# Optimization experiments

Hardware: AMD Instinct MI355X
Metric: run time of the kernel (lower is better)

Reference implementation:

```python
import jax, jax.numpy as jnp
import numpy as np

N, D, H, E, OUT, TOP_K = 16384, 1024, 4096, 8, 4096, 2


def setup_inputs() -> dict:
    key = jax.random.key(0)
    ks = jax.random.split(key, 9)
    s_d = 1.0 / np.sqrt(D)
    s_h = 1.0 / np.sqrt(H)
    return {
        "x": jax.random.normal(ks[0], (N, D), dtype=jnp.float32),
        "W_in": jax.random.normal(ks[1], (D, D), dtype=jnp.float32) * s_d,
        "b_in": jax.random.normal(ks[2], (D,), dtype=jnp.float32) * 0.01,
        "W_gate": jax.random.normal(ks[3], (D, E), dtype=jnp.float32) * s_d,
        "W1": jax.random.normal(ks[4], (E, D, H), dtype=jnp.float32) * s_d,
        "b1": jax.random.normal(ks[5], (E, H), dtype=jnp.float32) * 0.01,
        "W2": jax.random.normal(ks[6], (E, H, D), dtype=jnp.float32) * s_h,
        "b2": jax.random.normal(ks[7], (E, D), dtype=jnp.float32) * 0.01,
        "W_head": jax.random.normal(ks[8], (D, OUT), dtype=jnp.float32) * s_d,
    }


def reference(x, W_in, b_in, W_gate, W1, b1, W2, b2, W_head):
    # Input linear: [N, D]
    h = x @ W_in + b_in

    # Gating: softmax over experts, keep top-k, renormalize
    probs = jax.nn.softmax(h @ W_gate, axis=-1)            # [N, E]
    top_vals, top_idx = jax.lax.top_k(probs, TOP_K)        # [N, K]
    top_vals = top_vals / jnp.sum(top_vals, axis=-1, keepdims=True)
    rows = jnp.arange(h.shape[0])[:, None]
    combine = jnp.zeros_like(probs).at[rows, top_idx].set(top_vals)  # [N, E]

    # Expert FFNs, weighted combine (loop over small fixed expert count)
    moe_out = jnp.zeros_like(h)
    for e in range(E):
        he = jax.nn.relu(h @ W1[e] + b1[e])                # [N, H]
        ye = he @ W2[e] + b2[e]                            # [N, D]
        moe_out = moe_out + combine[:, e:e + 1] * ye

    # Head (no bias)
    return moe_out @ W_head
```

## Files before the change

### kernel.cpp

```cpp
#include <hip/hip_runtime.h>
#include <math.h>

#define NN 16384
#define DD 1024
#define HH 4096
#define EE 8
#define OUTD 4096

typedef unsigned short u16;
typedef short v8s __attribute__((ext_vector_type(8)));
typedef float v4f __attribute__((ext_vector_type(4)));

__device__ __forceinline__ u16 f2bf(float f) {
    unsigned int u = __float_as_uint(f);
    u = (u + 0x7fffu + ((u >> 16) & 1u)) >> 16;
    return (u16)u;
}

__device__ __forceinline__ void cp16(const u16* g, u16* l) {
    __builtin_amdgcn_global_load_lds(
        (const __attribute__((address_space(1))) unsigned int*)g,
        (__attribute__((address_space(3))) unsigned int*)l, 16, 0, 0);
}

__global__ __launch_bounds__(256) void cvt_bf16(const float* __restrict__ in,
                                                u16* __restrict__ out, int n4) {
    int i = blockIdx.x * 256 + threadIdx.x;
    if (i < n4) {
        float4 v = ((const float4*)in)[i];
        ushort4 o;
        o.x = f2bf(v.x); o.y = f2bf(v.y); o.z = f2bf(v.z); o.w = f2bf(v.w);
        ((ushort4*)out)[i] = o;
    }
}

__global__ __launch_bounds__(256) void transpose_cast(const float* __restrict__ in,
                                                      u16* __restrict__ out,
                                                      int rows, int cols) {
    __shared__ float t[32][33];
    const float* inp = in + (size_t)blockIdx.z * rows * cols;
    u16* outp = out + (size_t)blockIdx.z * rows * cols;
    int c0 = blockIdx.x * 32, r0 = blockIdx.y * 32;
    int tx = threadIdx.x & 31, ty = threadIdx.x >> 5;
#pragma unroll
    for (int i = 0; i < 4; ++i)
        t[ty + i * 8][tx] = inp[(size_t)(r0 + ty + i * 8) * cols + c0 + tx];
    __syncthreads();
#pragma unroll
    for (int i = 0; i < 4; ++i)
        outp[(size_t)(c0 + ty + i * 8) * rows + r0 + tx] = f2bf(t[tx][ty + i * 8]);
}

__global__ __launch_bounds__(256) void compute_G(const float* __restrict__ Win,
                                                 const float* __restrict__ Wg,
                                                 const float* __restrict__ b_in,
                                                 float* __restrict__ Gt,
                                                 float* __restrict__ cvec) {
    int tid = blockIdx.x * 256 + threadIdx.x;
    if (tid < EE * DD) {
        int e = tid >> 10, d = tid & 1023;
        float s = 0.f;
        for (int j = 0; j < DD; ++j) s += Win[(size_t)d * DD + j] * Wg[j * EE + e];
        Gt[e * DD + d] = s;
    } else if (tid < EE * DD + EE) {
        int e = tid - EE * DD;
        float s = 0.f;
        for (int j = 0; j < DD; ++j) s += b_in[j] * Wg[j * EE + e];
        cvec[e] = s;
    }
}

__global__ __launch_bounds__(256) void gate_kernel(const float* __restrict__ x,
                                                   const float* __restrict__ Gt,
                                                   const float* __restrict__ cvec,
                                                   int* __restrict__ counts,
                                                   int* __restrict__ toklist,
                                                   float* __restrict__ wtlist) {
    int wave = threadIdx.x >> 6, lane = threadIdx.x & 63;
    int t = blockIdx.x * 4 + wave;
    const float* xr = x + (size_t)t * DD;
    float p[EE];
#pragma unroll
    for (int e = 0; e < EE; ++e) p[e] = 0.f;
    for (int it = 0; it < DD / 64; ++it) {
        int d = it * 64 + lane;
        float xv = xr[d];
#pragma unroll
        for (int e = 0; e < EE; ++e) p[e] += xv * Gt[e * DD + d];
    }
#pragma unroll
    for (int e = 0; e < EE; ++e) {
        float v = p[e];
#pragma unroll
        for (int m = 32; m >= 1; m >>= 1) v += __shfl_xor(v, m);
        p[e] = v;
    }
    if (lane == 0) {
        float l[EE];
#pragma unroll
        for (int e = 0; e < EE; ++e) l[e] = p[e] + cvec[e];
        int i0 = 0; float v0 = l[0];
#pragma unroll
        for (int e = 1; e < EE; ++e) if (l[e] > v0) { v0 = l[e]; i0 = e; }
        int i1 = -1; float v1 = -1e30f;
#pragma unroll
        for (int e = 0; e < EE; ++e) if (e != i0 && l[e] > v1) { v1 = l[e]; i1 = e; }
        float e1 = __expf(v1 - v0);
        float inv = 1.f / (1.f + e1);
        float w0 = inv, w1 = e1 * inv;
        int pos0 = atomicAdd(&counts[i0], 1);
        toklist[i0 * NN + pos0] = t; wtlist[i0 * NN + pos0] = w0;
        int pos1 = atomicAdd(&counts[i1], 1);
        toklist[i1 * NN + pos1] = t; wtlist[i1 * NN + pos1] = w1;
    }
}

__global__ void offsets_kernel(const int* __restrict__ counts, int* __restrict__ offs) {
    if (threadIdx.x == 0) {
        int a = 0;
        for (int e = 0; e < EE; ++e) { offs[e] = a; a += counts[e]; }
    }
}

template <int MODE, int K, int LDC>
__global__ __launch_bounds__(256, 2) void gemm_bt(
    const u16* __restrict__ A, const u16* __restrict__ Btb,
    u16* __restrict__ outb, float* __restrict__ outf,
    const float* __restrict__ biasb,
    const int* __restrict__ toklist, const float* __restrict__ wtlist,
    const int* __restrict__ counts, const int* __restrict__ offsets,
    float* __restrict__ moe) {
    __shared__ __align__(16) u16 As[3][128 * 32];
    __shared__ __align__(16) u16 Bs[3][128 * 32];

    constexpr int GX = (MODE == 1 || MODE == 2) ? EE * 128 : NN / 128;
    constexpr int GY = LDC / 128;
    constexpr int NWG = GX * GY;
    constexpr int QC = NWG / 8;
    static_assert(NWG % 8 == 0, "xcd swizzle needs nwg%8==0");

    const int wg = blockIdx.x + GX * blockIdx.y;
    const int lid = (wg & 7) * QC + (wg >> 3);
    const int bx = lid & (GX - 1);
    const int by = lid / GX;

    int e = 0, mt = bx, cnt = 0, ofs = 0;
    if (MODE == 1 || MODE == 2) {
        e = bx >> 7; mt = bx & 127;
        cnt = counts[e];
        if (mt * 128 >= cnt) return;
        ofs = offsets[e];
    }
    const int m0 = mt * 128;
    const int n0 = by * 128;

    const u16* Bt = Btb;
    const float* bias = biasb;
    if (MODE == 1) { Bt += (size_t)e * HH * DD; bias += e * HH; }
    if (MODE == 2) { Bt += (size_t)e * DD * HH; bias += e * DD; }

    const int lane = threadIdx.x & 63;
    const int wave = threadIdx.x >> 6;
    const int rl = lane >> 2;
    const int kc = lane & 3;
    const int kcs = kc ^ ((rl >> 1) & 3);

    const u16* aS[2];
    const u16* bS[2];
#pragma unroll
    for (int s = 0; s < 2; ++s) {
        int trow = wave * 32 + s * 16 + rl;
        long arow;
        if (MODE == 1) {
            int rr = m0 + trow; if (rr >= cnt) rr = cnt - 1;
            arow = toklist[e * NN + rr];
        } else if (MODE == 2) {
            int rr = m0 + trow; if (rr >= cnt) rr = cnt - 1;
            arow = ofs + rr;
        } else {
            arow = m0 + trow;
        }
        aS[s] = A + (size_t)arow * K + kcs * 8;
        bS[s] = Bt + (size_t)(n0 + trow) * K + kcs * 8;
    }
    u16* aL[2] = { &As[0][(wave * 32) * 32], &As[0][(wave * 32 + 16) * 32] };
    u16* bL[2] = { &Bs[0][(wave * 32) * 32], &Bs[0][(wave * 32 + 16) * 32] };

    const int wm = wave & 1, wn = wave >> 1;
    const int fr = lane & 15;
    const int kswz = ((lane >> 4) ^ ((fr >> 1) & 3)) * 8;

    v4f acc[4][4];
#pragma unroll
    for (int i = 0; i < 4; ++i)
#pragma unroll
        for (int j = 0; j < 4; ++j)
#pragma unroll
            for (int c = 0; c < 4; ++c) acc[i][j][c] = 0.f;

    auto STAGE = [&](int kt, int buf) {
#pragma unroll
        for (int s = 0; s < 2; ++s) {
            cp16(aS[s] + kt * 32, aL[s] + buf * 4096);
            cp16(bS[s] + kt * 32, bL[s] + buf * 4096);
        }
    };

    constexpr int NIT = K / 32;
    STAGE(0, 0);
    STAGE(1, 1);

    int cur = 0, pre = 2;
    for (int it = 0; it < NIT; ++it) {
        if (it + 2 < NIT) {
            STAGE(it + 2, pre);
            asm volatile("s_waitcnt vmcnt(8)" ::: "memory");
        } else if (it + 2 == NIT) {
            asm volatile("s_waitcnt vmcnt(4)" ::: "memory");
        } else {
            asm volatile("s_waitcnt vmcnt(0)" ::: "memory");
        }
        __builtin_amdgcn_s_barrier();
        asm volatile("" ::: "memory");

        v8s af[4], bv[4];
#pragma unroll
        for (int i = 0; i < 4; ++i)
            af[i] = *(const v8s*)&As[cur][(wm * 64 + i * 16 + fr) * 32 + kswz];
#pragma unroll
        for (int j = 0; j < 4; ++j)
            bv[j] = *(const v8s*)&Bs[cur][(wn * 64 + j * 16 + fr) * 32 + kswz];

        __builtin_amdgcn_s_setprio(1);
#pragma unroll
        for (int i = 0; i < 4; ++i)
#pragma unroll
            for (int j = 0; j < 4; ++j)
                acc[i][j] = __builtin_amdgcn_mfma_f32_16x16x32_bf16(af[i], bv[j], acc[i][j], 0, 0, 0);
        __builtin_amdgcn_s_setprio(0);

        asm volatile("" ::: "memory");
        __builtin_amdgcn_s_barrier();
        cur = cur == 2 ? 0 : cur + 1;
        pre = pre == 2 ? 0 : pre + 1;
    }

    const int quad = (lane >> 4) * 4;
#pragma unroll
    for (int i = 0; i < 4; ++i) {
#pragma unroll
        for (int r = 0; r < 4; ++r) {
            int rloc = wm * 64 + i * 16 + quad + r;
            int grow = m0 + rloc;
            if ((MODE == 1 || MODE == 2) && grow >= cnt) continue;
            int tok = 0; float wgt = 0.f;
            if (MODE == 2) { tok = toklist[e * NN + grow]; wgt = wtlist[e * NN + grow]; }
#pragma unroll
            for (int j = 0; j < 4; ++j) {
                int col = n0 + wn * 64 + j * 16 + fr;
                float v = acc[i][j][r];
                if (MODE == 0) {
                    outb[(size_t)grow * LDC + col] = f2bf(v + bias[col]);
                } else if (MODE == 1) {
                    float t = v + bias[col];
                    t = t > 0.f ? t : 0.f;
                    outb[(size_t)(ofs + grow) * LDC + col] = f2bf(t);
                } else if (MODE == 2) {
                    atomicAdd(&moe[(size_t)tok * LDC + col], wgt * (v + bias[col]));
                } else {
                    outf[(size_t)grow * LDC + col] = v;
                }
            }
        }
    }
}

extern "C" void kernel_launch(void* const* d_in, const int* in_sizes, int n_in,
                              void* d_out, int out_size, void* d_ws, size_t ws_size,
                              hipStream_t stream) {
    const float* x    = (const float*)d_in[0];
    const float* Win  = (const float*)d_in[1];
    const float* b_in = (const float*)d_in[2];
    const float* Wg   = (const float*)d_in[3];
    const float* W1   = (const float*)d_in[4];
    const float* b1   = (const float*)d_in[5];
    const float* W2   = (const float*)d_in[6];
    const float* b2   = (const float*)d_in[7];
    const float* Wh   = (const float*)d_in[8];
    float* out = (float*)d_out;

    char* p = (char*)d_ws;
    size_t off = 0;
    auto alloc = [&](size_t bytes) {
        char* r = p + off;
        off = (off + bytes + 255) & ~(size_t)255;
        return r;
    };
    u16*   x_bf   = (u16*)alloc((size_t)NN * DD * 2);
    u16*   wint   = (u16*)alloc((size_t)DD * DD * 2);
    u16*   w1t    = (u16*)alloc((size_t)EE * DD * HH * 2);
    u16*   w2t    = (u16*)alloc((size_t)EE * DD * HH * 2);
    u16*   wht    = (u16*)alloc((size_t)DD * OUTD * 2);
    u16*   h_bf   = (u16*)alloc((size_t)NN * DD * 2);
    float* moe_f  = (float*)alloc((size_t)NN * DD * 4);
    u16*   moe_bf = (u16*)alloc((size_t)NN * DD * 2);
    float* Gt     = (float*)alloc((size_t)EE * DD * 4);
    float* cvec   = (float*)alloc(256);
    int*   counts = (int*)alloc(256);
    int*   offs   = (int*)alloc(256);
    int*   tok    = (int*)alloc((size_t)EE * NN * 4);
    float* wt     = (float*)alloc((size_t)EE * NN * 4);
    if (off > ws_size) return;

    u16* he = (u16*)d_out;

    hipMemsetAsync(counts, 0, 256, stream);
    hipMemsetAsync(moe_f, 0, (size_t)NN * DD * 4, stream);

    cvt_bf16<<<dim3(NN * DD / 4 / 256), 256, 0, stream>>>(x, x_bf, NN * DD / 4);
    transpose_cast<<<dim3(DD / 32, DD / 32, 1), 256, 0, stream>>>(Win, wint, DD, DD);
    transpose_cast<<<dim3(HH / 32, DD / 32, EE), 256, 0, stream>>>(W1, w1t, DD, HH);
    transpose_cast<<<dim3(DD / 32, HH / 32, EE), 256, 0, stream>>>(W2, w2t, HH, DD);
    transpose_cast<<<dim3(OUTD / 32, DD / 32, 1), 256, 0, stream>>>(Wh, wht, DD, OUTD);
    compute_G<<<dim3((EE * DD + EE + 255) / 256), 256, 0, stream>>>(Win, Wg, b_in, Gt, cvec);

    gemm_bt<0, DD, DD><<<dim3(NN / 128, DD / 128), 256, 0, stream>>>(
        x_bf, wint, h_bf, nullptr, b_in, nullptr, nullptr, nullptr, nullptr, nullptr);

    gate_kernel<<<dim3(NN / 4), 256, 0, stream>>>(x, Gt, cvec, counts, tok, wt);
    offsets_kernel<<<dim3(1), 64, 0, stream>>>(counts, offs);

    gemm_bt<1, DD, HH><<<dim3(EE * 128, HH / 128), 256, 0, stream>>>(
        h_bf, w1t, he, nullptr, b1, tok, wt, counts, offs, nullptr);

    gemm_bt<2, HH, DD><<<dim3(EE * 128, DD / 128), 256, 0, stream>>>(
        he, w2t, nullptr, nullptr, b2, tok, wt, counts, offs, moe_f);

    cvt_bf16<<<dim3(NN * DD / 4 / 256), 256, 0, stream>>>(moe_f, moe_bf, NN * DD / 4);

    gemm_bt<3, DD, OUTD><<<dim3(NN / 128, OUTD / 128), 256, 0, stream>>>(
        moe_bf, wht, nullptr, out, nullptr, nullptr, nullptr, nullptr, nullptr, nullptr);
}
```

Baseline: 2.170 ms.

## Parallelize compute_G per wave, raise GEMM occupancy, rework XCD tile swizzle

Rewrites compute_G so each wave computes one output with a lane-strided dot product and a shuffle reduction, replacing a serial 1024-long loop per thread with strided row reads. Raises the gemm_bt launch bound from 2 to 3 blocks per SM to allow more resident waves, at the risk of register pressure and spills. Replaces the XCD swizzle with a mode-dependent mapping that gives each XCD a contiguous chunk of M tiles (modes 0/2) or N stripes (modes 1/3), so each XCD's L2 reuses one operand.

```diff
diff --git a/kernel.cpp b/kernel.cpp
--- a/kernel.cpp
+++ b/kernel.cpp
@@ -56,17 +56,30 @@
                                                  const float* __restrict__ b_in,
                                                  float* __restrict__ Gt,
                                                  float* __restrict__ cvec) {
-    int tid = blockIdx.x * 256 + threadIdx.x;
-    if (tid < EE * DD) {
-        int e = tid >> 10, d = tid & 1023;
+    int wid = (blockIdx.x * 256 + threadIdx.x) >> 6;
+    int lane = threadIdx.x & 63;
+    if (wid < EE * DD) {
+        int e = wid >> 10, d = wid & 1023;
         float s = 0.f;
-        for (int j = 0; j < DD; ++j) s += Win[(size_t)d * DD + j] * Wg[j * EE + e];
-        Gt[e * DD + d] = s;
-    } else if (tid < EE * DD + EE) {
-        int e = tid - EE * DD;
+#pragma unroll
+        for (int i = 0; i < DD / 64; ++i) {
+            int j = i * 64 + lane;
+            s += Win[(size_t)d * DD + j] * Wg[j * EE + e];
+        }
+#pragma unroll
+        for (int m = 32; m >= 1; m >>= 1) s += __shfl_xor(s, m);
+        if (lane == 0) Gt[e * DD + d] = s;
+    } else if (wid < EE * DD + EE) {
+        int e = wid - EE * DD;
         float s = 0.f;
-        for (int j = 0; j < DD; ++j) s += b_in[j] * Wg[j * EE + e];
-        cvec[e] = s;
+#pragma unroll
+        for (int i = 0; i < DD / 64; ++i) {
+            int j = i * 64 + lane;
+            s += b_in[j] * Wg[j * EE + e];
+        }
+#pragma unroll
+        for (int m = 32; m >= 1; m >>= 1) s += __shfl_xor(s, m);
+        if (lane == 0) cvec[e] = s;
     }
 }
 
@@ -123,7 +136,7 @@
 }
 
 template <int MODE, int K, int LDC>
-__global__ __launch_bounds__(256, 2) void gemm_bt(
+__global__ __launch_bounds__(256, 3) void gemm_bt(
     const u16* __restrict__ A, const u16* __restrict__ Btb,
     u16* __restrict__ outb, float* __restrict__ outf,
     const float* __restrict__ biasb,
@@ -135,14 +148,24 @@
 
     constexpr int GX = (MODE == 1 || MODE == 2) ? EE * 128 : NN / 128;
     constexpr int GY = LDC / 128;
-    constexpr int NWG = GX * GY;
-    constexpr int QC = NWG / 8;
-    static_assert(NWG % 8 == 0, "xcd swizzle needs nwg%8==0");
+    static_assert(GX % 8 == 0 && GY % 8 == 0 || (MODE == 1 || MODE == 3),
+                  "swizzle divisibility");
 
     const int wg = blockIdx.x + GX * blockIdx.y;
-    const int lid = (wg & 7) * QC + (wg >> 3);
-    const int bx = lid & (GX - 1);
-    const int by = lid / GX;
+    const int c = wg & 7;
+    const int q = wg >> 3;
+    int bx, by;
+    if (MODE == 0 || MODE == 2) {
+        constexpr int CW = GX / 8;
+        static_assert(GX % 8 == 0, "bx-chunk needs GX%8==0");
+        bx = c * CW + q / GY;
+        by = q % GY;
+    } else {
+        constexpr int SH = GY / 8;
+        static_assert(GY % 8 == 0, "by-stripe needs GY%8==0");
+        bx = q / SH;
+        by = c * SH + q % SH;
+    }
 
     int e = 0, mt = bx, cnt = 0, ofs = 0;
     if (MODE == 1 || MODE == 2) {
@@ -196,7 +219,7 @@
 #pragma unroll
         for (int j = 0; j < 4; ++j)
 #pragma unroll
-            for (int c = 0; c < 4; ++c) acc[i][j][c] = 0.f;
+            for (int c2 = 0; c2 < 4; ++c2) acc[i][j][c2] = 0.f;
 
     auto STAGE = [&](int kt, int buf) {
 #pragma unroll
@@ -322,7 +345,7 @@
     transpose_cast<<<dim3(HH / 32, DD / 32, EE), 256, 0, stream>>>(W1, w1t, DD, HH);
     transpose_cast<<<dim3(DD / 32, HH / 32, EE), 256, 0, stream>>>(W2, w2t, HH, DD);
     transpose_cast<<<dim3(OUTD / 32, DD / 32, 1), 256, 0, stream>>>(Wh, wht, DD, OUTD);
-    compute_G<<<dim3((EE * DD + EE + 255) / 256), 256, 0, stream>>>(Win, Wg, b_in, Gt, cvec);
+    compute_G<<<dim3((EE * DD + EE) / 4), 256, 0, stream>>>(Win, Wg, b_in, Gt, cvec);
 
     gemm_bt<0, DD, DD><<<dim3(NN / 128, DD / 128), 256, 0, stream>>>(
         x_bf, wint, h_bf, nullptr, b_in, nullptr, nullptr, nullptr, nullptr, nullptr);
```

Result: faster. 2.006 ms (-7.5%).
